# Kernel optimization log

Measured on AMD Instinct MI355X. Metric: run time of the kernel, lower is better.

## Reference

```python
import jax, jax.numpy as jnp
from jax import lax
import numpy as np

BINS = 25
K = 5  # entropy patch size
EPS = 1e-5


def conv2d(x, w, b, stride, pad):
    y = lax.conv_general_dilated(x, w, (stride, stride), [(pad, pad), (pad, pad)],
                                 dimension_numbers=("NCHW", "OIHW", "NCHW"))
    return y + b[None, :, None, None]


def group_norm_per_channel(x, w, b):
    # GroupNorm with num_groups == num_channels: per-channel norm over H,W (biased var)
    mu = x.mean(axis=(2, 3), keepdims=True)
    v = x.var(axis=(2, 3), keepdims=True)
    return (x - mu) / jnp.sqrt(v + EPS) * w[None, :, None, None] + b[None, :, None, None]


def channel_entropy(x):
    # x: (b,c,h,w). Unfold into 5x5 patches, per-patch histc(bins=25) over patch
    # values using that patch's min/max range (torch.histc default), then entropy.
    b, c, h, w = x.shape
    ho, wo = h - K + 1, w - K + 1
    # (b,c,K*K,L) -- fixed 25-position loop, vectorized over all data dims
    patches = jnp.stack([x[:, :, i:i + ho, j:j + wo]
                         for i in range(K) for j in range(K)], axis=2)
    patches = patches.reshape(b, c, K * K, ho * wo)
    mn = patches.min(axis=2, keepdims=True)
    mx = patches.max(axis=2, keepdims=True)
    rng = jnp.where(mx > mn, mx - mn, jnp.ones_like(mx))
    bins = jnp.clip(jnp.floor((patches - mn) / rng * BINS), 0, BINS - 1).astype(jnp.int32)
    # histogram via comparison one-hot: (b,c,L,BINS)
    counts = (bins[..., None] == jnp.arange(BINS, dtype=jnp.int32)).sum(axis=2)
    pk = counts.astype(x.dtype) / (K * K)
    ent = (-pk * jnp.log(jnp.clip(pk, 1e-5, 1.0 - 1e-5))).sum(axis=-1).mean(axis=-1)  # (b,c)
    return ent[:, :, None, None]


def instance_norm_ent(x, w, b):
    ent = channel_entropy(lax.stop_gradient(x))
    mu = x.mean(axis=(2, 3), keepdims=True)
    n = x.shape[2] * x.shape[3]
    v = x.var(axis=(2, 3), keepdims=True) * (n / (n - 1))  # unbiased var (torch default)
    return (x - mu) / jnp.sqrt(v + EPS) * w[None, :, None, None] * ent + b[None, :, None, None]


def setup_inputs() -> dict:
    key = jax.random.key(0)
    ks = jax.random.split(key, 24)
    s = 0.05
    d = {
        "x": jax.random.normal(ks[0], (64, 3, 224, 224), jnp.float32),
        "conv0_w": jax.random.normal(ks[1], (8, 3, 7, 7), jnp.float32) * s,
        "conv0_b": jax.random.normal(ks[2], (8,), jnp.float32) * s,
        "conv1_w": jax.random.normal(ks[3], (16, 8, 5, 5), jnp.float32) * s,
        "conv1_b": jax.random.normal(ks[4], (16,), jnp.float32) * s,
        "conv2_w": jax.random.normal(ks[5], (32, 16, 3, 3), jnp.float32) * s,
        "conv2_b": jax.random.normal(ks[6], (32,), jnp.float32) * s,
        "gn0_w": jnp.ones((8,), jnp.float32) + jax.random.normal(ks[7], (8,), jnp.float32) * s,
        "gn0_b": jax.random.normal(ks[8], (8,), jnp.float32) * s,
        "n1_w": jnp.ones((16,), jnp.float32) + jax.random.normal(ks[9], (16,), jnp.float32) * s,
        "n1_b": jax.random.normal(ks[10], (16,), jnp.float32) * s,
        "n2_w": jnp.ones((32,), jnp.float32) + jax.random.normal(ks[11], (32,), jnp.float32) * s,
        "n2_b": jax.random.normal(ks[12], (32,), jnp.float32) * s,
        "bn_g": jnp.ones((10368,), jnp.float32) + jax.random.normal(ks[13], (10368,), jnp.float32) * s,
        "bn_b": jax.random.normal(ks[14], (10368,), jnp.float32) * s,
        "fc1_w": jax.random.normal(ks[15], (32, 10368), jnp.float32) * 0.01,
        "fc1_b": jax.random.normal(ks[16], (32,), jnp.float32) * s,
        "shape_w": jax.random.normal(ks[17], (5, 32), jnp.float32) * s,
        "shape_b": jax.random.normal(ks[18], (5,), jnp.float32) * s,
        "vern_w": jax.random.normal(ks[19], (2, 32), jnp.float32) * s,
        "vern_b": jax.random.normal(ks[20], (2,), jnp.float32) * s,
    }
    return d


def reference(x, conv0_w, conv0_b, conv1_w, conv1_b, conv2_w, conv2_b,
              gn0_w, gn0_b, n1_w, n1_b, n2_w, n2_b,
              bn_g, bn_b, fc1_w, fc1_b, shape_w, shape_b, vern_w, vern_b):
    h = conv2d(x, conv0_w, conv0_b, 4, 2)          # (b,8,56,56)
    h = jax.nn.relu(group_norm_per_channel(h, gn0_w, gn0_b))
    h = conv2d(h, conv1_w, conv1_b, 3, 1)          # (b,16,18,18)
    h = jax.nn.relu(instance_norm_ent(h, n1_w, n1_b))
    h = conv2d(h, conv2_w, conv2_b, 1, 1)          # (b,32,18,18)
    h = jax.nn.relu(instance_norm_ent(h, n2_w, n2_b))
    h = h.reshape(h.shape[0], -1)                  # (b,10368)
    # BatchNorm1d (training mode: batch stats, biased var)
    mu = h.mean(axis=0)
    v = h.var(axis=0)
    h = (h - mu) / jnp.sqrt(v + EPS) * bn_g + bn_b
    h = jax.nn.relu(h @ fc1_w.T + fc1_b)           # (b,32)
    out_shape = jax.nn.softmax(h @ shape_w.T + shape_b, axis=-1)
    out_vern = jax.nn.softmax(h @ vern_w.T + vern_b, axis=-1)
    return (out_shape, out_vern)
```

## Files before the change

kernel.cpp:

```cpp
#include <hip/hip_runtime.h>
#include <math.h>

#define EPSD 1e-5


__device__ __forceinline__ double waveReduceSumD(double v) {
#pragma unroll
    for (int off = 32; off > 0; off >>= 1)
        v += __shfl_down(v, off, 64);
    return v;
}

template <int NW>
__device__ __forceinline__ double blockReduceSumD(double v, double* buf) {
    int lane = threadIdx.x & 63;
    int w = threadIdx.x >> 6;
    v = waveReduceSumD(v);
    __syncthreads();
    if (lane == 0) buf[w] = v;
    __syncthreads();
    double tot = 0.0;
#pragma unroll
    for (int i = 0; i < NW; i++) tot += buf[i];
    return tot;
}

__device__ __forceinline__ void build_ent_tab(float* tab) {
    int t = threadIdx.x;
    if (t < 26) {
        if (t == 0) tab[0] = 0.f;
        else {
            double pk = (double)t / 25.0;
            double cl = fmin(fmax(pk, 1e-5), 1.0 - 1e-5);
            tab[t] = (float)(-pk * log(cl));
        }
    }
}

__device__ __forceinline__ float patch_ent(const float* ch, int py, int px, const float* tab) {
    float pv[25];
#pragma unroll
    for (int i = 0; i < 5; i++)
#pragma unroll
        for (int j = 0; j < 5; j++)
            pv[i * 5 + j] = ch[(py + i) * 18 + px + j];
    float mn = pv[0], mx = pv[0];
#pragma unroll
    for (int k = 1; k < 25; k++) { mn = fminf(mn, pv[k]); mx = fmaxf(mx, pv[k]); }
    float rng = (mx > mn) ? (mx - mn) : 1.0f;
    float scl = 25.0f / rng;
    unsigned long long a0 = 0ull, a1 = 0ull;
    int a2 = 0;
#pragma unroll
    for (int k = 0; k < 25; k++) {
        float tt = (pv[k] - mn) * scl;
        int bi = (int)floorf(tt);
        bi = bi < 0 ? 0 : (bi > 24 ? 24 : bi);
        unsigned sh0 = ((unsigned)(5 * bi)) & 63u;
        unsigned sh1 = ((unsigned)(5 * bi - 60)) & 63u;
        a0 += (bi < 12) ? (1ull << sh0) : 0ull;
        a1 += (bi >= 12 && bi < 24) ? (1ull << sh1) : 0ull;
        a2 += (bi == 24) ? 1 : 0;
    }
    float ent = 0.f;
#pragma unroll
    for (int k = 0; k < 12; k++) ent += tab[(a0 >> (5 * k)) & 31ull];
#pragma unroll
    for (int k = 0; k < 12; k++) ent += tab[(a1 >> (5 * k)) & 31ull];
    ent += tab[a2];
    return ent;
}

__global__ __launch_bounds__(128, 4) void k_conv0(const float* __restrict__ x,
                                                  const float* __restrict__ w,
                                                  const float* __restrict__ bias,
                                                  float* __restrict__ h0raw,
                                                  double* __restrict__ part0) {
    __shared__ __align__(16) float tile[2508];
    __shared__ double redbuf[2][16];
    int tl = blockIdx.x;
    int b = blockIdx.y;
    int t = threadIdx.x;
    for (int i = t; i < 2508; i += 128) tile[i] = 0.f;
    int y_base = tl * 8 - 2;
    const float* xb = x + (size_t)b * 150528;
    float acc[8];
#pragma unroll
    for (int c = 0; c < 8; c++) acc[c] = bias[c];
    int ry = t / 56, ox = t % 56;
    for (int ci = 0; ci < 3; ci++) {
        __syncthreads();
        for (int i = t; i < 616; i += 128) {
            int r = i / 56, f4 = i % 56;
            int yIn = y_base + r;
            if (yIn >= 0 && yIn < 224) {
                float4 v = *(const float4*)&xb[ci * 50176 + yIn * 224 + f4 * 4];
                float* tp = tile + r * 228;
                tp[114 + f4] = v.x;
                tp[171 + f4] = v.y;
                tp[f4 + 1]   = v.z;
                tp[58 + f4]  = v.w;
            }
        }
        __syncthreads();
        if (t < 112) {
            const float* wci = w + ci * 49;
#pragma unroll 1
            for (int ky = 0; ky < 7; ky++) {
                const float* rp = tile + (4 * ry + ky) * 228;
#pragma unroll
                for (int kx = 0; kx < 7; kx++) {
                    float v = rp[(kx & 3) * 57 + ox + (kx >> 2)];
#pragma unroll
                    for (int c = 0; c < 8; c++)
                        acc[c] += v * wci[c * 147 + ky * 7 + kx];
                }
            }
        }
    }
    if (t < 112) {
        int oy = tl * 2 + ry;
        int opix = oy * 56 + ox;
#pragma unroll
        for (int c = 0; c < 8; c++)
            h0raw[((size_t)b * 8 + c) * 3136 + opix] = acc[c];
    } else {
#pragma unroll
        for (int c = 0; c < 8; c++) acc[c] = 0.f;
    }
    int wv = t >> 6, lane = t & 63;
#pragma unroll
    for (int c = 0; c < 8; c++) {
        double rs = waveReduceSumD((double)acc[c]);
        double rq = waveReduceSumD((double)acc[c] * (double)acc[c]);
        if (lane == 0) { redbuf[wv][c * 2] = rs; redbuf[wv][c * 2 + 1] = rq; }
    }
    __syncthreads();
    if (t < 16) {
        double tot = redbuf[0][t] + redbuf[1][t];
        part0[(((size_t)b * 28 + tl) << 4) + t] = tot;
    }
}

__global__ __launch_bounds__(1024) void k_conv1_ent(const float* __restrict__ h0raw,
                                                    const double* __restrict__ part0,
                                                    const float* __restrict__ gw,
                                                    const float* __restrict__ gb,
                                                    const float* __restrict__ w,
                                                    const float* __restrict__ bias,
                                                    const float* __restrict__ nw,
                                                    const float* __restrict__ nb,
                                                    float* __restrict__ h1) {
    __shared__ __align__(16) float xin2[25088];
    __shared__ float vals[1296];
    __shared__ float tab[26];
    __shared__ float gnp[16];
    __shared__ double redbuf[16][2];
    __shared__ double entbuf[16];
    __shared__ float prm[4][3];
    int b = blockIdx.x >> 2;
    int grp = blockIdx.x & 3;
    int t = threadIdx.x;
    if (t < 8) {
        double s = 0.0, s2 = 0.0;
        const double* p = part0 + ((size_t)b * 28) * 16;
        for (int tile = 0; tile < 28; tile++) {
            s += p[tile * 16 + t * 2];
            s2 += p[tile * 16 + t * 2 + 1];
        }
        double mean = s / 3136.0;
        double var = s2 / 3136.0 - mean * mean;
        double rstd = 1.0 / sqrt(var + EPSD);
        double sc = (double)gw[t] * rstd;
        gnp[t] = (float)sc;
        gnp[8 + t] = (float)((double)gb[t] - mean * sc);
    }
    build_ent_tab(tab);
    __syncthreads();
    for (int i4 = t; i4 < 6272; i4 += 1024) {
        int ci = i4 / 784;
        int px = (i4 - ci * 784) * 4;
        float4 v4 = *(const float4*)&h0raw[(size_t)b * 25088 + ci * 3136 + px];
        float gs = gnp[ci], gh = gnp[8 + ci];
        float* dst = xin2 + (ci >> 1) * 6272 + px * 2 + (ci & 1);
        dst[0] = fmaxf(v4.x * gs + gh, 0.f);
        dst[2] = fmaxf(v4.y * gs + gh, 0.f);
        dst[4] = fmaxf(v4.z * gs + gh, 0.f);
        dst[6] = fmaxf(v4.w * gs + gh, 0.f);
    }
    __syncthreads();

    int wv = t >> 6, lane = t & 63;
    int c = wv >> 2;
    int q = wv & 3;
    int j_u = __builtin_amdgcn_readfirstlane(grp * 4 + c);
    const float* wg = w + (size_t)j_u * 200;
    float* vch = vals + c * 324;
    float bv = bias[j_u];
    double s = 0.0, s2 = 0.0;
    for (int p = q * 81 + lane; p < q * 81 + 81; p += 64) {
        int oy = p / 18, ox = p - oy * 18;
        int y0 = oy * 3 - 1, x0 = ox * 3 - 1;
        float acc = bv;
        if (oy >= 1 && ox >= 1) {
#pragma unroll
            for (int c2 = 0; c2 < 4; c2++) {
                const float* xp = xin2 + c2 * 6272 + (y0 * 56 + x0) * 2;
                const float* wp0 = wg + (2 * c2) * 25;
#pragma unroll
                for (int ky = 0; ky < 5; ky++)
#pragma unroll
                    for (int kx = 0; kx < 5; kx++) {
                        float2 v = *(const float2*)&xp[(ky * 56 + kx) * 2];
                        acc += v.x * wp0[ky * 5 + kx];
                        acc += v.y * wp0[25 + ky * 5 + kx];
                    }
            }
        } else {
            int ky0 = y0 < 0 ? 1 : 0;
            int kx0 = x0 < 0 ? 1 : 0;
            for (int c2 = 0; c2 < 4; c2++) {
                const float* xp = xin2 + c2 * 6272;
                const float* wp0 = wg + (2 * c2) * 25;
                for (int ky = ky0; ky < 5; ky++) {
                    for (int kx = kx0; kx < 5; kx++) {
                        float2 v = *(const float2*)&xp[((y0 + ky) * 56 + x0 + kx) * 2];
                        acc += v.x * wp0[ky * 5 + kx];
                        acc += v.y * wp0[25 + ky * 5 + kx];
                    }
                }
            }
        }
        vch[p] = acc;
        s += (double)acc; s2 += (double)acc * (double)acc;
    }
    s = waveReduceSumD(s);
    s2 = waveReduceSumD(s2);
    if (lane == 0) { redbuf[wv][0] = s; redbuf[wv][1] = s2; }
    __syncthreads();
    double ent = 0.0;
    if (lane < 49) {
        int pi = q * 49 + lane;
        ent = (double)patch_ent(vch, pi / 14, pi % 14, tab);
    }
    ent = waveReduceSumD(ent);
    if (lane == 0) entbuf[wv] = ent;
    __syncthreads();
    if (t < 4) {
        double ss = 0.0, qq = 0.0, ee = 0.0;
        for (int k = 0; k < 4; k++) {
            ss += redbuf[t * 4 + k][0];
            qq += redbuf[t * 4 + k][1];
            ee += entbuf[t * 4 + k];
        }
        double entmean = ee / 196.0;
        double mean = ss / 324.0;
        double varb = qq / 324.0 - mean * mean;
        double varu = varb * (324.0 / 323.0);
        double rstd = 1.0 / sqrt(varu + EPSD);
        prm[t][0] = (float)mean;
        prm[t][1] = (float)((double)nw[grp * 4 + t] * entmean * rstd);
        prm[t][2] = nb[grp * 4 + t];
    }
    __syncthreads();
    float* outp = h1 + ((size_t)b * 16 + grp * 4) * 324;
    for (int i = t; i < 1296; i += 1024) {
        int cc = i / 324;
        outp[i] = fmaxf((vals[i] - prm[cc][0]) * prm[cc][1] + prm[cc][2], 0.f);
    }
}

__global__ __launch_bounds__(256) void k_conv2_ent(const float* __restrict__ in,
                                                   const float* __restrict__ w,
                                                   const float* __restrict__ bias,
                                                   const float* __restrict__ nw,
                                                   const float* __restrict__ nb,
                                                   float* __restrict__ out) {
    __shared__ __align__(16) float xin2[5184];
    __shared__ float vals[324];
    __shared__ float tab[26];
    __shared__ double rbuf[4];
    int b = blockIdx.x >> 5;
    int c = blockIdx.x & 31;
    int t = threadIdx.x;
    const float* xb = in + (size_t)b * 5184;
    for (int i4 = t; i4 < 1296; i4 += 256) {
        int ci = i4 / 81;
        int px = (i4 - ci * 81) * 4;
        float4 v4 = *(const float4*)&xb[ci * 324 + px];
        float* dst = xin2 + (ci >> 1) * 648 + px * 2 + (ci & 1);
        dst[0] = v4.x; dst[2] = v4.y; dst[4] = v4.z; dst[6] = v4.w;
    }
    build_ent_tab(tab);
    __syncthreads();
    const float* wc = w + c * 144;
    float bv = bias[c];
    double s = 0.0, s2 = 0.0;
    {
        int oy = 1 + (t >> 4), ox = 1 + (t & 15);
        int base = ((oy - 1) * 18 + (ox - 1)) * 2;
        float acc = bv;
#pragma unroll
        for (int c2 = 0; c2 < 8; c2++) {
            const float* xp = xin2 + c2 * 648 + base;
            const float* wp = wc + c2 * 18;
#pragma unroll
            for (int ky = 0; ky < 3; ky++)
#pragma unroll
                for (int kx = 0; kx < 3; kx++) {
                    float2 v = *(const float2*)&xp[(ky * 18 + kx) * 2];
                    acc += v.x * wp[ky * 3 + kx];
                    acc += v.y * wp[9 + ky * 3 + kx];
                }
        }
        vals[oy * 18 + ox] = acc;
        s += (double)acc; s2 += (double)acc * (double)acc;
    }
    if (t < 68) {
        int oy, ox;
        if (t < 18)      { oy = 0;      ox = t; }
        else if (t < 36) { oy = 17;     ox = t - 18; }
        else if (t < 52) { oy = t - 35; ox = 0; }
        else             { oy = t - 51; ox = 17; }
        int y0 = oy - 1, x0 = ox - 1;
        int ky0 = y0 < 0 ? 1 : 0;
        int ky1 = (18 - y0) < 3 ? 2 : 3;
        int kx0 = x0 < 0 ? 1 : 0;
        int kx1 = (18 - x0) < 3 ? 2 : 3;
        float acc = bv;
        for (int c2 = 0; c2 < 8; c2++) {
            const float* xp = xin2 + c2 * 648;
            const float* wp = wc + c2 * 18;
            for (int ky = ky0; ky < ky1; ky++) {
                for (int kx = kx0; kx < kx1; kx++) {
                    float2 v = *(const float2*)&xp[((y0 + ky) * 18 + x0 + kx) * 2];
                    acc += v.x * wp[ky * 3 + kx];
                    acc += v.y * wp[9 + ky * 3 + kx];
                }
            }
        }
        vals[oy * 18 + ox] = acc;
        s += (double)acc; s2 += (double)acc * (double)acc;
    }
    __syncthreads();
    double ent = 0.0;
    if (t < 196) ent = (double)patch_ent(vals, t / 14, t % 14, tab);
    double entmean = blockReduceSumD<4>(ent, rbuf) / 196.0;
    double ssum  = blockReduceSumD<4>(s, rbuf);
    double s2sum = blockReduceSumD<4>(s2, rbuf);
    double mean = ssum / 324.0;
    double varb = s2sum / 324.0 - mean * mean;
    double varu = varb * (324.0 / 323.0);
    double rstd = 1.0 / sqrt(varu + EPSD);
    float sc = (float)((double)nw[c] * entmean * rstd);
    float mu = (float)mean;
    float be = nb[c];
    float* outp = out + ((size_t)b * 32 + c) * 324;
    for (int idx = t; idx < 324; idx += 256)
        outp[idx] = fmaxf((vals[idx] - mu) * sc + be, 0.f);
}

__global__ __launch_bounds__(256) void k_bnstats(const float* __restrict__ h2,
                                                 const float* __restrict__ g,
                                                 const float* __restrict__ bb,
                                                 float* __restrict__ hv) {
    __shared__ double sb[4][64], qb[4][64];
    __shared__ float scsh[2][64];
    int lane = threadIdx.x & 63;
    int q = threadIdx.x >> 6;
    int f = blockIdx.x * 64 + lane;
    double s = 0.0, s2 = 0.0;
    for (int b = q * 16; b < q * 16 + 16; b++) {
        double v = (double)h2[(size_t)b * 10368 + f];
        s += v; s2 += v * v;
    }
    sb[q][lane] = s; qb[q][lane] = s2;
    __syncthreads();
    if (threadIdx.x < 64) {
        double S = sb[0][lane] + sb[1][lane] + sb[2][lane] + sb[3][lane];
        double Q = qb[0][lane] + qb[1][lane] + qb[2][lane] + qb[3][lane];
        double mean = S / 64.0;
        double var = Q / 64.0 - mean * mean;
        double rstd = 1.0 / sqrt(var + EPSD);
        double sc = (double)g[f] * rstd;
        scsh[0][lane] = (float)sc;
        scsh[1][lane] = (float)((double)bb[f] - mean * sc);
    }
    __syncthreads();
    float sc = scsh[0][lane], sh = scsh[1][lane];
    for (int b = q * 16; b < q * 16 + 16; b++)
        hv[(size_t)b * 10368 + f] = h2[(size_t)b * 10368 + f] * sc + sh;
}

__global__ __launch_bounds__(256) void k_fc1(const float* __restrict__ hv,
                                             const float* __restrict__ w1,
                                             const float* __restrict__ b1,
                                             float* __restrict__ fcout) {
    __shared__ double rbuf[4];
    int b = blockIdx.x >> 5;
    int j = blockIdx.x & 31;
    const float* hb = hv + (size_t)b * 10368;
    const float* wj = w1 + (size_t)j * 10368;
    double acc = 0.0;
    for (int f = threadIdx.x * 4; f < 10368; f += 1024) {
        float4 h4 = *(const float4*)&hb[f];
        float4 w4 = *(const float4*)&wj[f];
        acc += (double)(h4.x * w4.x);
        acc += (double)(h4.y * w4.y);
        acc += (double)(h4.z * w4.z);
        acc += (double)(h4.w * w4.w);
    }
    acc = blockReduceSumD<4>(acc, rbuf);
    if (threadIdx.x == 0)
        fcout[b * 32 + j] = (float)fmax(acc + (double)b1[j], 0.0);
}

__global__ __launch_bounds__(64) void k_heads(const float* __restrict__ fc,
                                              const float* __restrict__ sw,
                                              const float* __restrict__ sb,
                                              const float* __restrict__ vw,
                                              const float* __restrict__ vb,
                                              float* __restrict__ out) {
    int b = threadIdx.x;
    double h[32];
#pragma unroll
    for (int i = 0; i < 32; i++) h[i] = (double)fc[b * 32 + i];
    double lg[5];
    double mx = -1e300;
#pragma unroll
    for (int k = 0; k < 5; k++) {
        double a = (double)sb[k];
#pragma unroll
        for (int i = 0; i < 32; i++) a += h[i] * (double)sw[k * 32 + i];
        lg[k] = a;
        mx = fmax(mx, a);
    }
    double se = 0.0;
#pragma unroll
    for (int k = 0; k < 5; k++) { lg[k] = exp(lg[k] - mx); se += lg[k]; }
#pragma unroll
    for (int k = 0; k < 5; k++) out[b * 5 + k] = (float)(lg[k] / se);
    double l0 = (double)vb[0], l1 = (double)vb[1];
#pragma unroll
    for (int i = 0; i < 32; i++) { l0 += h[i] * (double)vw[i]; l1 += h[i] * (double)vw[32 + i]; }
    double m = fmax(l0, l1);
    double e0 = exp(l0 - m), e1 = exp(l1 - m);
    double inv = 1.0 / (e0 + e1);
    out[320 + b * 2 + 0] = (float)(e0 * inv);
    out[320 + b * 2 + 1] = (float)(e1 * inv);
}

extern "C" void kernel_launch(void* const* d_in, const int* in_sizes, int n_in,
                              void* d_out, int out_size, void* d_ws, size_t ws_size,
                              hipStream_t stream) {
    const float* x       = (const float*)d_in[0];
    const float* conv0_w = (const float*)d_in[1];
    const float* conv0_b = (const float*)d_in[2];
    const float* conv1_w = (const float*)d_in[3];
    const float* conv1_b = (const float*)d_in[4];
    const float* conv2_w = (const float*)d_in[5];
    const float* conv2_b = (const float*)d_in[6];
    const float* gn0_w   = (const float*)d_in[7];
    const float* gn0_b   = (const float*)d_in[8];
    const float* n1_w    = (const float*)d_in[9];
    const float* n1_b    = (const float*)d_in[10];
    const float* n2_w    = (const float*)d_in[11];
    const float* n2_b    = (const float*)d_in[12];
    const float* bn_g    = (const float*)d_in[13];
    const float* bn_b    = (const float*)d_in[14];
    const float* fc1_w   = (const float*)d_in[15];
    const float* fc1_b   = (const float*)d_in[16];
    const float* shape_w = (const float*)d_in[17];
    const float* shape_b = (const float*)d_in[18];
    const float* vern_w  = (const float*)d_in[19];
    const float* vern_b  = (const float*)d_in[20];
    float* out = (float*)d_out;

    double* part0 = (double*)d_ws;
    float* fbase   = (float*)(part0 + 28672);
    float* h0raw   = fbase;
    float* h1      = h0raw + 1605632;
    float* h2      = h1 + 331776;
    float* hv      = h2 + 663552;
    float* fc      = hv + 663552;

    k_conv0<<<dim3(28, 64), dim3(128), 0, stream>>>(x, conv0_w, conv0_b, h0raw, part0);
    k_conv1_ent<<<dim3(256), dim3(1024), 0, stream>>>(h0raw, part0, gn0_w, gn0_b,
                                                      conv1_w, conv1_b, n1_w, n1_b, h1);
    k_conv2_ent<<<dim3(2048), dim3(256), 0, stream>>>(h1, conv2_w, conv2_b, n2_w, n2_b, h2);
    k_bnstats<<<dim3(162), dim3(256), 0, stream>>>(h2, bn_g, bn_b, hv);
    k_fc1<<<dim3(2048), dim3(256), 0, stream>>>(hv, fc1_w, fc1_b, fc);
    k_heads<<<dim3(1), dim3(64), 0, stream>>>(fc, shape_w, shape_b, vern_w, vern_b, out);
}
```

Baseline: 212.5 us.

## Compute two output channels per block in conv2+entropy kernel

Each conv2 block now produces two output channels for one batch sample, using 512 threads and half as many blocks. The staged, interleaved input tile is loaded once and reused for both channels, and each input value feeds two accumulators. Per-channel reductions are merged into a single wave-level pass with one final combine, and the two channels' entropy work runs on separate thread ranges. In exchange each block uses more threads and registers, and some threads sit idle in the conv phase (324 of 512 active), which may hurt occupancy.

```diff
diff --git a/kernel.cpp b/kernel.cpp
--- a/kernel.cpp
+++ b/kernel.cpp
@@ -270,21 +270,24 @@
     }
 }
 
-__global__ __launch_bounds__(256) void k_conv2_ent(const float* __restrict__ in,
+__global__ __launch_bounds__(512) void k_conv2_ent(const float* __restrict__ in,
                                                    const float* __restrict__ w,
                                                    const float* __restrict__ bias,
                                                    const float* __restrict__ nw,
                                                    const float* __restrict__ nb,
                                                    float* __restrict__ out) {
     __shared__ __align__(16) float xin2[5184];
-    __shared__ float vals[324];
+    __shared__ float vals[648];
     __shared__ float tab[26];
-    __shared__ double rbuf[4];
-    int b = blockIdx.x >> 5;
-    int c = blockIdx.x & 31;
+    __shared__ double redbuf[8][4];
+    __shared__ double entbuf[8];
+    __shared__ float prm[2][3];
+    int b = blockIdx.x >> 4;
+    int pr = blockIdx.x & 15;
+    int c0 = pr * 2, c1 = c0 + 1;
     int t = threadIdx.x;
     const float* xb = in + (size_t)b * 5184;
-    for (int i4 = t; i4 < 1296; i4 += 256) {
+    for (int i4 = t; i4 < 1296; i4 += 512) {
         int ci = i4 / 81;
         int px = (i4 - ci * 81) * 4;
         float4 v4 = *(const float4*)&xb[ci * 324 + px];
@@ -293,71 +296,104 @@
     }
     build_ent_tab(tab);
     __syncthreads();
-    const float* wc = w + c * 144;
-    float bv = bias[c];
-    double s = 0.0, s2 = 0.0;
-    {
+    const float* wc0 = w + c0 * 144;
+    const float* wc1 = w + c1 * 144;
+    float acc0 = 0.f, acc1 = 0.f;
+    if (t < 256) {
         int oy = 1 + (t >> 4), ox = 1 + (t & 15);
         int base = ((oy - 1) * 18 + (ox - 1)) * 2;
-        float acc = bv;
+        acc0 = bias[c0]; acc1 = bias[c1];
 #pragma unroll
         for (int c2 = 0; c2 < 8; c2++) {
             const float* xp = xin2 + c2 * 648 + base;
-            const float* wp = wc + c2 * 18;
+            const float* wp0 = wc0 + c2 * 18;
+            const float* wp1 = wc1 + c2 * 18;
 #pragma unroll
             for (int ky = 0; ky < 3; ky++)
 #pragma unroll
                 for (int kx = 0; kx < 3; kx++) {
                     float2 v = *(const float2*)&xp[(ky * 18 + kx) * 2];
-                    acc += v.x * wp[ky * 3 + kx];
-                    acc += v.y * wp[9 + ky * 3 + kx];
+                    acc0 += v.x * wp0[ky * 3 + kx];
+                    acc0 += v.y * wp0[9 + ky * 3 + kx];
+                    acc1 += v.x * wp1[ky * 3 + kx];
+                    acc1 += v.y * wp1[9 + ky * 3 + kx];
                 }
         }
-        vals[oy * 18 + ox] = acc;
-        s += (double)acc; s2 += (double)acc * (double)acc;
-    }
-    if (t < 68) {
+        vals[oy * 18 + ox] = acc0;
+        vals[324 + oy * 18 + ox] = acc1;
+    } else if (t < 324) {
+        int bid = t - 256;
         int oy, ox;
-        if (t < 18)      { oy = 0;      ox = t; }
-        else if (t < 36) { oy = 17;     ox = t - 18; }
-        else if (t < 52) { oy = t - 35; ox = 0; }
-        else             { oy = t - 51; ox = 17; }
+        if (bid < 18)      { oy = 0;        ox = bid; }
+        else if (bid < 36) { oy = 17;       ox = bid - 18; }
+        else if (bid < 52) { oy = bid - 35; ox = 0; }
+        else               { oy = bid - 51; ox = 17; }
         int y0 = oy - 1, x0 = ox - 1;
         int ky0 = y0 < 0 ? 1 : 0;
         int ky1 = (18 - y0) < 3 ? 2 : 3;
         int kx0 = x0 < 0 ? 1 : 0;
         int kx1 = (18 - x0) < 3 ? 2 : 3;
-        float acc = bv;
+        acc0 = bias[c0]; acc1 = bias[c1];
         for (int c2 = 0; c2 < 8; c2++) {
             const float* xp = xin2 + c2 * 648;
-            const float* wp = wc + c2 * 18;
+            const float* wp0 = wc0 + c2 * 18;
+            const float* wp1 = wc1 + c2 * 18;
             for (int ky = ky0; ky < ky1; ky++) {
                 for (int kx = kx0; kx < kx1; kx++) {
                     float2 v = *(const float2*)&xp[((y0 + ky) * 18 + x0 + kx) * 2];
-                    acc += v.x * wp[ky * 3 + kx];
-                    acc += v.y * wp[9 + ky * 3 + kx];
+                    acc0 += v.x * wp0[ky * 3 + kx];
+                    acc0 += v.y * wp0[9 + ky * 3 + kx];
+                    acc1 += v.x * wp1[ky * 3 + kx];
+                    acc1 += v.y * wp1[9 + ky * 3 + kx];
                 }
             }
         }
-        vals[oy * 18 + ox] = acc;
-        s += (double)acc; s2 += (double)acc * (double)acc;
+        vals[oy * 18 + ox] = acc0;
+        vals[324 + oy * 18 + ox] = acc1;
+    }
+    int wv = t >> 6, lane = t & 63;
+    {
+        double s0 = waveReduceSumD((double)acc0);
+        double q0 = waveReduceSumD((double)acc0 * (double)acc0);
+        double s1 = waveReduceSumD((double)acc1);
+        double q1 = waveReduceSumD((double)acc1 * (double)acc1);
+        if (lane == 0) {
+            redbuf[wv][0] = s0; redbuf[wv][1] = q0;
+            redbuf[wv][2] = s1; redbuf[wv][3] = q1;
+        }
     }
     __syncthreads();
     double ent = 0.0;
     if (t < 196) ent = (double)patch_ent(vals, t / 14, t % 14, tab);
-    double entmean = blockReduceSumD<4>(ent, rbuf) / 196.0;
-    double ssum  = blockReduceSumD<4>(s, rbuf);
-    double s2sum = blockReduceSumD<4>(s2, rbuf);
-    double mean = ssum / 324.0;
-    double varb = s2sum / 324.0 - mean * mean;
-    double varu = varb * (324.0 / 323.0);
-    double rstd = 1.0 / sqrt(varu + EPSD);
-    float sc = (float)((double)nw[c] * entmean * rstd);
-    float mu = (float)mean;
-    float be = nb[c];
-    float* outp = out + ((size_t)b * 32 + c) * 324;
-    for (int idx = t; idx < 324; idx += 256)
-        outp[idx] = fmaxf((vals[idx] - mu) * sc + be, 0.f);
+    else if (t >= 256 && t < 452) {
+        int pi = t - 256;
+        ent = (double)patch_ent(vals + 324, pi / 14, pi % 14, tab);
+    }
+    ent = waveReduceSumD(ent);
+    if (lane == 0) entbuf[wv] = ent;
+    __syncthreads();
+    if (t < 2) {
+        double ss = 0.0, qq = 0.0, ee = 0.0;
+        for (int k = 0; k < 8; k++) {
+            ss += redbuf[k][t * 2];
+            qq += redbuf[k][t * 2 + 1];
+        }
+        for (int k = 0; k < 4; k++) ee += entbuf[t * 4 + k];
+        double entmean = ee / 196.0;
+        double mean = ss / 324.0;
+        double varb = qq / 324.0 - mean * mean;
+        double varu = varb * (324.0 / 323.0);
+        double rstd = 1.0 / sqrt(varu + EPSD);
+        prm[t][0] = (float)mean;
+        prm[t][1] = (float)((double)nw[c0 + t] * entmean * rstd);
+        prm[t][2] = nb[c0 + t];
+    }
+    __syncthreads();
+    float* outp = out + ((size_t)b * 32 + c0) * 324;
+    for (int i = t; i < 648; i += 512) {
+        int cc = i / 324;
+        outp[i] = fmaxf((vals[i] - prm[cc][0]) * prm[cc][1] + prm[cc][2], 0.f);
+    }
 }
 
 __global__ __launch_bounds__(256) void k_bnstats(const float* __restrict__ h2,
@@ -487,7 +523,7 @@
     k_conv0<<<dim3(28, 64), dim3(128), 0, stream>>>(x, conv0_w, conv0_b, h0raw, part0);
     k_conv1_ent<<<dim3(256), dim3(1024), 0, stream>>>(h0raw, part0, gn0_w, gn0_b,
                                                       conv1_w, conv1_b, n1_w, n1_b, h1);
-    k_conv2_ent<<<dim3(2048), dim3(256), 0, stream>>>(h1, conv2_w, conv2_b, n2_w, n2_b, h2);
+    k_conv2_ent<<<dim3(1024), dim3(512), 0, stream>>>(h1, conv2_w, conv2_b, n2_w, n2_b, h2);
     k_bnstats<<<dim3(162), dim3(256), 0, stream>>>(h2, bn_g, bn_b, hv);
     k_fc1<<<dim3(2048), dim3(256), 0, stream>>>(hv, fc1_w, fc1_b, fc);
     k_heads<<<dim3(1), dim3(64), 0, stream>>>(fc, shape_w, shape_b, vern_w, vern_b, out);
```

New measurement: 210.8 us. No clear change (-0.8%).
